# Performance work log

Hardware: AMD Instinct MI355X
Metric: run time of the kernel (lower is better)

## Reference

```python
import jax, jax.numpy as jnp
import numpy as np
from jax import lax


def setup_inputs() -> dict:
    key = jax.random.key(0)
    B, S, D = 32, 2048, 1024
    k1, = jax.random.split(key, 1)
    hidden = jax.random.normal(k1, (B, S, D), dtype=jnp.float32)
    mask = jnp.ones((B, S), dtype=jnp.int64)
    x = 64
    return {"hidden": hidden, "mask": mask, "x": x}


def reference(hidden, mask, x):
    # Faithful to the torch forward: the python loop overwrites ht each
    # iteration, so only the LAST sample's session length matters, and the
    # slice is taken over the FULL batch (hidden[:, ...], not hidden[i]).
    B, S, D = hidden.shape
    session_lengths = jnp.sum(mask, axis=1)          # [B]
    length = session_lengths[B - 1]                  # last sample's length
    start = length - x                               # dynamic start, static width x
    window = lax.dynamic_slice(hidden, (0, start.astype(jnp.int32), 0), (B, x, D))  # [B, x, D]
    ht = jnp.sum(window, axis=1)                     # [B, D]
    return ht
```

## Files before the change

kernel.cpp:

```cpp
#include <hip/hip_runtime.h>

__global__ __launch_bounds__(256) void srs_window_sum(
    const float4* __restrict__ hidden,
    const int* __restrict__ mask,
    const int* __restrict__ xp,
    float* __restrict__ out,
    int B, int S, int D4, int jsplit)
{
    __shared__ int s_wave[4];
    __shared__ int s_start;
    const int tid = threadIdx.x;
    const int x = *xp;

    int acc = 0;
    const int* mrow = mask + (size_t)(B - 1) * S;
    for (int i = tid; i < S; i += 256) acc += mrow[i];
    #pragma unroll
    for (int off = 32; off > 0; off >>= 1) acc += __shfl_down(acc, off, 64);
    if ((tid & 63) == 0) s_wave[tid >> 6] = acc;
    __syncthreads();
    if (tid == 0) {
        int length = s_wave[0] + s_wave[1] + s_wave[2] + s_wave[3];
        int start = length - x;
        if (start < 0) start = 0;
        if (start > S - x) start = S - x;
        s_start = start;
    }
    __syncthreads();
    const int start = s_start;

    const int gid = blockIdx.x * 256 + tid;
    if (gid >= B * D4) return;
    const int b = gid / D4;
    const int d = gid - b * D4;

    const int chunk = (x + jsplit - 1) / jsplit;
    const int j0 = blockIdx.y * chunk;
    int j1 = j0 + chunk; if (j1 > x) j1 = x;

    const float4* p = hidden + ((size_t)b * S + (size_t)start) * D4 + d;
    float4 s = make_float4(0.f, 0.f, 0.f, 0.f);
    for (int j = j0; j < j1; ++j) {
        float4 h = p[(size_t)j * D4];
        s.x += h.x; s.y += h.y; s.z += h.z; s.w += h.w;
    }

    float* o = out + (size_t)gid * 4;
    atomicAdd(o + 0, s.x);
    atomicAdd(o + 1, s.y);
    atomicAdd(o + 2, s.z);
    atomicAdd(o + 3, s.w);
}

extern "C" void kernel_launch(void* const* d_in, const int* in_sizes, int n_in,
                              void* d_out, int out_size, void* d_ws, size_t ws_size,
                              hipStream_t stream) {
    const float* hidden = (const float*)d_in[0];
    const int*   mask   = (const int*)d_in[1];
    const int*   xp     = (const int*)d_in[2];
    float*       out    = (float*)d_out;

    const long long nhid  = in_sizes[0];
    const long long nmask = in_sizes[1];
    const int D  = (int)(nhid / nmask);
    const int S  = (int)(nhid / (long long)out_size);
    const int B  = out_size / D;
    const int D4 = D / 4;

    hipMemsetAsync(d_out, 0, (size_t)out_size * sizeof(float), stream);

    const int jsplit = 8;
    dim3 grid((B * D4 + 255) / 256, jsplit);
    srs_window_sum<<<grid, 256, 0, stream>>>(
        (const float4*)hidden, mask, xp, out, B, S, D4, jsplit);
}
```

Measured before the change: 300.9 us.

## Reduce window splits in shared memory and drop atomics and memset

Replaces the grid-level split over the window (8 y-blocks with float atomics into a zeroed output) with one block per (batch, 64-float4 tile), where four waves each sum a quarter of the window and combine through shared memory before a single float4 store. This removes the hipMemsetAsync launch and all global atomics. The mask row is also read with int4 loads. The trade-off is a smaller grid (B*4 blocks) with less parallelism per output, and every block still re-reduces the mask row.

```diff
diff --git a/kernel.cpp b/kernel.cpp
--- a/kernel.cpp
+++ b/kernel.cpp
@@ -1,23 +1,38 @@
 #include <hip/hip_runtime.h>
+
+#define JQ 4
 
 __global__ __launch_bounds__(256) void srs_window_sum(
     const float4* __restrict__ hidden,
     const int* __restrict__ mask,
     const int* __restrict__ xp,
-    float* __restrict__ out,
-    int B, int S, int D4, int jsplit)
+    float4* __restrict__ out,
+    int B, int S, int D4, int ntile)
 {
-    __shared__ int s_wave[4];
+    __shared__ int s_wave[JQ];
     __shared__ int s_start;
-    const int tid = threadIdx.x;
-    const int x = *xp;
+    __shared__ float4 s_part[256];
+
+    const int tid  = threadIdx.x;
+    const int lane = tid & 63;
+    const int w    = tid >> 6;
+    const int x    = *xp;
 
     int acc = 0;
     const int* mrow = mask + (size_t)(B - 1) * S;
-    for (int i = tid; i < S; i += 256) acc += mrow[i];
+    if ((S & 3) == 0) {
+        const int4* m4 = (const int4*)mrow;
+        const int S4 = S >> 2;
+        for (int i = tid; i < S4; i += 256) {
+            int4 v = m4[i];
+            acc += v.x + v.y + v.z + v.w;
+        }
+    } else {
+        for (int i = tid; i < S; i += 256) acc += mrow[i];
+    }
     #pragma unroll
     for (int off = 32; off > 0; off >>= 1) acc += __shfl_down(acc, off, 64);
-    if ((tid & 63) == 0) s_wave[tid >> 6] = acc;
+    if (lane == 0) s_wave[w] = acc;
     __syncthreads();
     if (tid == 0) {
         int length = s_wave[0] + s_wave[1] + s_wave[2] + s_wave[3];
@@ -29,27 +44,37 @@
     __syncthreads();
     const int start = s_start;
 
-    const int gid = blockIdx.x * 256 + tid;
-    if (gid >= B * D4) return;
-    const int b = gid / D4;
-    const int d = gid - b * D4;
+    const int b    = blockIdx.x / ntile;
+    const int tile = blockIdx.x - b * ntile;
+    const int d4   = tile * 64 + lane;
 
-    const int chunk = (x + jsplit - 1) / jsplit;
-    const int j0 = blockIdx.y * chunk;
+    const int chunk = (x + JQ - 1) / JQ;
+    const int j0 = w * chunk;
     int j1 = j0 + chunk; if (j1 > x) j1 = x;
 
-    const float4* p = hidden + ((size_t)b * S + (size_t)start) * D4 + d;
     float4 s = make_float4(0.f, 0.f, 0.f, 0.f);
-    for (int j = j0; j < j1; ++j) {
-        float4 h = p[(size_t)j * D4];
-        s.x += h.x; s.y += h.y; s.z += h.z; s.w += h.w;
+    if (d4 < D4) {
+        const float4* p = hidden + ((size_t)b * S + (size_t)start) * D4 + d4;
+        for (int j = j0; j < j1; ++j) {
+            float4 h = p[(size_t)j * D4];
+            s.x += h.x; s.y += h.y; s.z += h.z; s.w += h.w;
+        }
     }
+    s_part[tid] = s;
+    __syncthreads();
 
-    float* o = out + (size_t)gid * 4;
-    atomicAdd(o + 0, s.x);
-    atomicAdd(o + 1, s.y);
-    atomicAdd(o + 2, s.z);
-    atomicAdd(o + 3, s.w);
+    if (tid < 64) {
+        float4 a = s_part[tid];
+        float4 b1 = s_part[tid + 64];
+        float4 c = s_part[tid + 128];
+        float4 d1 = s_part[tid + 192];
+        float4 r;
+        r.x = a.x + b1.x + c.x + d1.x;
+        r.y = a.y + b1.y + c.y + d1.y;
+        r.z = a.z + b1.z + c.z + d1.z;
+        r.w = a.w + b1.w + c.w + d1.w;
+        if (d4 < D4) out[(size_t)b * D4 + d4] = r;
+    }
 }
 
 extern "C" void kernel_launch(void* const* d_in, const int* in_sizes, int n_in,
@@ -58,7 +83,7 @@
     const float* hidden = (const float*)d_in[0];
     const int*   mask   = (const int*)d_in[1];
     const int*   xp     = (const int*)d_in[2];
-    float*       out    = (float*)d_out;
+    float4*      out    = (float4*)d_out;
 
     const long long nhid  = in_sizes[0];
     const long long nmask = in_sizes[1];
@@ -67,10 +92,8 @@
     const int B  = out_size / D;
     const int D4 = D / 4;
 
-    hipMemsetAsync(d_out, 0, (size_t)out_size * sizeof(float), stream);
-
-    const int jsplit = 8;
-    dim3 grid((B * D4 + 255) / 256, jsplit);
+    const int ntile = (D4 + 63) / 64;
+    dim3 grid(B * ntile);
     srs_window_sum<<<grid, 256, 0, stream>>>(
-        (const float4*)hidden, mask, xp, out, B, S, D4, jsplit);
+        (const float4*)hidden, mask, xp, out, B, S, D4, ntile);
 }
```

After: 301.5 us. Within noise of the previous version (+0.2%).
